# Optimization experiments

Hardware: AMD Instinct MI355X
Metric: run time of the kernel (lower is better)

## Reference

```python
import jax, jax.numpy as jnp
import numpy as np


def setup_inputs() -> dict:
    key = jax.random.key(0)
    ks = jax.random.split(key, 8)
    B, T, U = 4, 256, 128
    De, Dp, D, V = 512, 512, 640, 1024
    s = lambda k, sh, fan: jax.random.normal(k, sh, dtype=jnp.float32) / np.sqrt(fan)
    return {
        "enc": jax.random.normal(ks[0], (B, T, De), dtype=jnp.float32),
        "pred": jax.random.normal(ks[1], (B, U, Dp), dtype=jnp.float32),
        "W_enc": s(ks[2], (De, D), De),
        "b_enc": jnp.zeros((D,), jnp.float32),
        "W_pred": s(ks[3], (Dp, D), Dp),
        "b_pred": jnp.zeros((D,), jnp.float32),
        "W_joint": s(ks[4], (D, V), D),
        "b_joint": jnp.zeros((V,), jnp.float32),
    }


def reference(enc, pred, W_enc, b_enc, W_pred, b_pred, W_joint, b_joint):
    # f: [B,T,D], g: [B,U,D]
    f = jnp.einsum("bte,ed->btd", enc, W_enc) + b_enc
    g = jnp.einsum("bup,pd->bud", pred, W_pred) + b_pred
    # broadcast-add over the T x U lattice, tanh activation
    joint = jnp.tanh(f[:, :, None, :] + g[:, None, :, :])  # [B,T,U,D]
    # final projection to num_classes
    out = jnp.einsum("btud,dv->btuv", joint, W_joint) + b_joint  # [B,T,U,V]
    return out
```

## Files before the change

kernel.cpp:

```cpp
#include <hip/hip_runtime.h>
#include <hip/hip_bf16.h>
#include <stdint.h>

typedef unsigned short u16;
typedef __attribute__((ext_vector_type(8))) __bf16 bf16x8;
typedef __attribute__((ext_vector_type(4))) float f32x4;
typedef __attribute__((ext_vector_type(16))) float f32x16;
typedef __attribute__((ext_vector_type(8))) unsigned short u16x8;
typedef __attribute__((ext_vector_type(4))) unsigned int u32x4;

static __device__ __forceinline__ u16 f2bf(float x) {
  __hip_bfloat16 h = __float2bfloat16(x);
  u16 u;
  __builtin_memcpy(&u, &h, 2);
  return u;
}

static __device__ __forceinline__ float fast_tanh(float x) {
  float e = __expf(2.0f * x);
  return 1.0f - 2.0f * __builtin_amdgcn_rcpf(e + 1.0f);
}

static __device__ __forceinline__ void gload_lds16(const void* g, void* l) {
  __builtin_amdgcn_global_load_lds(
      (const __attribute__((address_space(1))) unsigned int*)g,
      (__attribute__((address_space(3))) unsigned int*)l, 16, 0, 0);
}

static __device__ __forceinline__ int swz(int row, int byte_in_row) {
  return row * 128 + (byte_in_row ^ ((row & 7) << 4));
}

__global__ __launch_bounds__(256) void transpose_cast_kernel(
    const float* __restrict__ in, u16* __restrict__ out, int K, int N) {
  int n = blockIdx.x;
  for (int k = threadIdx.x; k < K; k += 256) {
    out[(size_t)n * K + k] = f2bf(in[(size_t)k * N + n]);
  }
}

__global__ __launch_bounds__(256) void linear_kernel(
    const float* __restrict__ A, const u16* __restrict__ Wt,
    const float* __restrict__ bias, float* __restrict__ out) {
  __shared__ u16 sA[64 * 64];
  __shared__ u16 sB[64 * 64];
  const int t = threadIdx.x;
  const int bx = blockIdx.x;
  const int m0 = (bx / 10) * 64;
  const int n0 = (bx % 10) * 64;
  const int lane = t & 63, wid = t >> 6;
  const int wr = wid >> 1, wc = wid & 1;
  const int l15 = lane & 15, lk8 = (lane >> 4) << 3;

  const int srow = t >> 2;
  const int kc = (t & 3) << 4;

  f32x4 acc[2][2] = {};

  for (int k0 = 0; k0 < 512; k0 += 64) {
    {
      const float4* gp = (const float4*)(A + (size_t)(m0 + srow) * 512 + k0 + kc);
      u16 tmp[16];
#pragma unroll
      for (int i = 0; i < 4; ++i) {
        float4 v = gp[i];
        tmp[i * 4 + 0] = f2bf(v.x);
        tmp[i * 4 + 1] = f2bf(v.y);
        tmp[i * 4 + 2] = f2bf(v.z);
        tmp[i * 4 + 3] = f2bf(v.w);
      }
      *(u16x8*)((char*)sA + swz(srow, kc * 2)) = *(u16x8*)&tmp[0];
      *(u16x8*)((char*)sA + swz(srow, kc * 2 + 16)) = *(u16x8*)&tmp[8];
    }
    {
      const int off = (t & 3) << 5;
      const char* gsrc = (const char*)Wt + ((size_t)(n0 + srow) * 512 + k0) * 2 + off;
      u32x4 q0 = *(const u32x4*)gsrc;
      u32x4 q1 = *(const u32x4*)(gsrc + 16);
      *(u32x4*)((char*)sB + swz(srow, off)) = q0;
      *(u32x4*)((char*)sB + swz(srow, off + 16)) = q1;
    }
    __syncthreads();
#pragma unroll
    for (int kh = 0; kh < 2; ++kh) {
      const int kbyte = kh * 64 + lk8 * 2;
      bf16x8 av[2], bv[2];
#pragma unroll
      for (int mf = 0; mf < 2; ++mf)
        av[mf] = *(const bf16x8*)((char*)sA + swz(wr * 32 + mf * 16 + l15, kbyte));
#pragma unroll
      for (int nf = 0; nf < 2; ++nf)
        bv[nf] = *(const bf16x8*)((char*)sB + swz(wc * 32 + nf * 16 + l15, kbyte));
#pragma unroll
      for (int mf = 0; mf < 2; ++mf)
#pragma unroll
        for (int nf = 0; nf < 2; ++nf)
          acc[mf][nf] = __builtin_amdgcn_mfma_f32_16x16x32_bf16(
              av[mf], bv[nf], acc[mf][nf], 0, 0, 0);
    }
    __syncthreads();
  }

  const int r4 = (lane >> 4) << 2;
#pragma unroll
  for (int nf = 0; nf < 2; ++nf) {
    const int nc = n0 + wc * 32 + nf * 16 + l15;
    const float bjv = bias[nc];
#pragma unroll
    for (int mf = 0; mf < 2; ++mf) {
      const int mr = m0 + wr * 32 + mf * 16 + r4;
#pragma unroll
      for (int r = 0; r < 4; ++r)
        out[(size_t)(mr + r) * 640 + nc] = acc[mf][nf][r] + bjv;
    }
  }
}

__global__ __launch_bounds__(256) void joint_kernel(
    const float* __restrict__ f, const float* __restrict__ g,
    u16* __restrict__ joint, int m_base) {
  int idx = blockIdx.x * 256 + threadIdx.x;
  int row = idx / 80;
  int kc = (idx % 80) * 8;
  int m = m_base + row;
  int bt = m >> 7;
  int b = bt >> 8;
  int u = m & 127;
  const float4* fp = (const float4*)(f + (size_t)bt * 640 + kc);
  const float4* gp = (const float4*)(g + ((size_t)(b * 128 + u)) * 640 + kc);
  u16 tmp[8];
#pragma unroll
  for (int i = 0; i < 2; ++i) {
    float4 fv = fp[i];
    float4 gv = gp[i];
    tmp[i * 4 + 0] = f2bf(fast_tanh(fv.x + gv.x));
    tmp[i * 4 + 1] = f2bf(fast_tanh(fv.y + gv.y));
    tmp[i * 4 + 2] = f2bf(fast_tanh(fv.z + gv.z));
    tmp[i * 4 + 3] = f2bf(fast_tanh(fv.w + gv.w));
  }
  *(u16x8*)(joint + (size_t)row * 640 + kc) = *(u16x8*)&tmp[0];
}

__global__ __launch_bounds__(512, 2) void gemm256_kernel(
    const u16* __restrict__ A,
    const u16* __restrict__ Bt,
    const float* __restrict__ bias,
    float* __restrict__ out,
    int m_base, int mtiles) {
  extern __shared__ char smem[];
  const int t = threadIdx.x;
  const int lane = t & 63, wid = t >> 6;

  const int nwg = mtiles * 4;
  const int bid = blockIdx.x;
  const int q = nwg >> 3, r = nwg & 7;
  const int xcd = bid & 7, local = bid >> 3;
  const int wgid = (xcd < r ? xcd * (q + 1) : r * (q + 1) + (xcd - r) * q) + local;
  const int mt = wgid >> 2, nt = wgid & 3;

  const int wr = wid >> 2, wc = wid & 3;
  const int l31 = lane & 31, hi = lane >> 5;
  const int rx = (lane & 7) << 4;

  const int srow = t >> 3;
  const int xc = ((t & 7) ^ ((t >> 3) & 7)) << 4;
  const u16* aSrc[4];
  const u16* bSrc[4];
#pragma unroll
  for (int j = 0; j < 4; ++j) {
    const int row = j * 64 + srow;
    aSrc[j] = A + (size_t)(mt * 256 + row) * 640 + (xc >> 1);
    bSrc[j] = Bt + (size_t)(nt * 256 + row) * 640 + (xc >> 1);
  }
  const int sdst = wid * 1024;

  f32x16 acc[4][2] = {};

#pragma unroll
  for (int j = 0; j < 4; ++j) {
    gload_lds16(aSrc[j], smem + j * 8192 + sdst);
    gload_lds16(bSrc[j], smem + 32768 + j * 8192 + sdst);
  }
  __syncthreads();

  for (int tt = 0; tt < 10; ++tt) {
    const int bufo = (tt & 1) * 65536;
    if (tt < 9) {
      const int ke = (tt + 1) * 64;
      const int nbufo = bufo ^ 65536;
#pragma unroll
      for (int j = 0; j < 4; ++j) {
        gload_lds16(aSrc[j] + ke, smem + nbufo + j * 8192 + sdst);
        gload_lds16(bSrc[j] + ke, smem + nbufo + 32768 + j * 8192 + sdst);
      }
    }
    const char* sA = smem + bufo;
    const char* sB = smem + bufo + 32768;
#pragma unroll
    for (int ks = 0; ks < 4; ++ks) {
      const int cb = (ks * 32 + (hi << 4)) ^ rx;
      bf16x8 bv[2], av[4];
#pragma unroll
      for (int nn = 0; nn < 2; ++nn)
        bv[nn] = *(const bf16x8*)(sB + (wc * 64 + nn * 32 + l31) * 128 + cb);
#pragma unroll
      for (int mm = 0; mm < 4; ++mm)
        av[mm] = *(const bf16x8*)(sA + (wr * 128 + mm * 32 + l31) * 128 + cb);
      __builtin_amdgcn_s_setprio(1);
#pragma unroll
      for (int mm = 0; mm < 4; ++mm)
#pragma unroll
        for (int nn = 0; nn < 2; ++nn)
          acc[mm][nn] = __builtin_amdgcn_mfma_f32_32x32x16_bf16(
              av[mm], bv[nn], acc[mm][nn], 0, 0, 0);
      __builtin_amdgcn_s_setprio(0);
    }
    if (tt < 9) __syncthreads();
  }

#pragma unroll
  for (int nn = 0; nn < 2; ++nn) {
    const int v = nt * 256 + wc * 64 + nn * 32 + l31;
    const float bjv = bias[v];
#pragma unroll
    for (int mm = 0; mm < 4; ++mm) {
      const size_t mrow =
          (size_t)m_base + (size_t)mt * 256 + wr * 128 + mm * 32 + hi * 4;
#pragma unroll
      for (int reg = 0; reg < 16; ++reg) {
        const int row = (reg & 3) + 8 * (reg >> 2);
        out[(mrow + row) * 1024 + v] = acc[mm][nn][reg] + bjv;
      }
    }
  }
}

__global__ __launch_bounds__(512) void fused_joint_kernel(
    const float* __restrict__ f, const float* __restrict__ g,
    const u16* __restrict__ Wjt, const float* __restrict__ bj,
    float* __restrict__ out) {
  __shared__ u16 sA[128 * 64];
  __shared__ u16 sB[256 * 64];
  const int t = threadIdx.x;
  const int bt = blockIdx.x;
  const int b = bt >> 8;
  const int v0 = blockIdx.y << 8;
  const float* frow = f + (size_t)bt * 640;
  const float* gbase = g + (size_t)b * 128 * 640;

  const int lane = t & 63, wid = t >> 6;
  const int wr = wid >> 2, wc = wid & 3;
  const int l15 = lane & 15, lk8 = (lane >> 4) << 3;

  const int au = t >> 2;
  const int akc = (t & 3) << 4;
  const int bn = t >> 1;
  const int boff = (t & 1) << 6;

  f32x4 acc[4][4] = {};

  for (int k0 = 0; k0 < 640; k0 += 64) {
    {
      const float4* gp = (const float4*)(gbase + (size_t)au * 640 + k0 + akc);
      const float4* fp = (const float4*)(frow + k0 + akc);
      u16 tmp[16];
#pragma unroll
      for (int i = 0; i < 4; ++i) {
        float4 gv = gp[i];
        float4 fv = fp[i];
        tmp[i * 4 + 0] = f2bf(fast_tanh(gv.x + fv.x));
        tmp[i * 4 + 1] = f2bf(fast_tanh(gv.y + fv.y));
        tmp[i * 4 + 2] = f2bf(fast_tanh(gv.z + fv.z));
        tmp[i * 4 + 3] = f2bf(fast_tanh(gv.w + fv.w));
      }
      *(u16x8*)((char*)sA + swz(au, akc * 2)) = *(u16x8*)&tmp[0];
      *(u16x8*)((char*)sA + swz(au, akc * 2 + 16)) = *(u16x8*)&tmp[8];
    }
    {
      const char* gsrc = (const char*)Wjt + ((size_t)(v0 + bn) * 640 + k0) * 2 + boff;
#pragma unroll
      for (int i = 0; i < 4; ++i) {
        u32x4 qv = *(const u32x4*)(gsrc + i * 16);
        *(u32x4*)((char*)sB + swz(bn, boff + i * 16)) = qv;
      }
    }
    __syncthreads();
#pragma unroll
    for (int kh = 0; kh < 2; ++kh) {
      const int kbyte = kh * 64 + lk8 * 2;
      bf16x8 av[4], bv[4];
#pragma unroll
      for (int mf = 0; mf < 4; ++mf)
        av[mf] = *(const bf16x8*)((char*)sA + swz(wr * 64 + mf * 16 + l15, kbyte));
#pragma unroll
      for (int nf = 0; nf < 4; ++nf)
        bv[nf] = *(const bf16x8*)((char*)sB + swz(wc * 64 + nf * 16 + l15, kbyte));
#pragma unroll
      for (int mf = 0; mf < 4; ++mf)
#pragma unroll
        for (int nf = 0; nf < 4; ++nf)
          acc[mf][nf] = __builtin_amdgcn_mfma_f32_16x16x32_bf16(
              av[mf], bv[nf], acc[mf][nf], 0, 0, 0);
    }
    __syncthreads();
  }

  const int r4 = (lane >> 4) << 2;
#pragma unroll
  for (int nf = 0; nf < 4; ++nf) {
    const int v = v0 + wc * 64 + nf * 16 + l15;
    const float bjv = bj[v];
#pragma unroll
    for (int mf = 0; mf < 4; ++mf) {
      const int u = wr * 64 + mf * 16 + r4;
      const size_t o = ((size_t)bt * 128 + u) * 1024 + v;
#pragma unroll
      for (int rr = 0; rr < 4; ++rr)
        out[o + (size_t)rr * 1024] = acc[mf][nf][rr] + bjv;
    }
  }
}

extern "C" void kernel_launch(void* const* d_in, const int* in_sizes, int n_in,
                              void* d_out, int out_size, void* d_ws, size_t ws_size,
                              hipStream_t stream) {
  const float* enc = (const float*)d_in[0];
  const float* pred = (const float*)d_in[1];
  const float* W_enc = (const float*)d_in[2];
  const float* b_enc = (const float*)d_in[3];
  const float* W_pred = (const float*)d_in[4];
  const float* b_pred = (const float*)d_in[5];
  const float* W_joint = (const float*)d_in[6];
  const float* b_joint = (const float*)d_in[7];
  float* out = (float*)d_out;

  char* ws = (char*)d_ws;
  float* f = (float*)ws;
  float* gbuf = (float*)(ws + 2621440);
  u16* Wet = (u16*)(ws + 2621440 + 1310720);
  u16* Wpt = (u16*)(ws + 2621440 + 1310720 + 655360);
  u16* Wjt = (u16*)(ws + 2621440 + 1310720 + 2 * 655360);
  const size_t fixed = 2621440 + 1310720 + 2 * 655360 + 1310720;
  u16* joint = (u16*)(ws + fixed);

  transpose_cast_kernel<<<640, 256, 0, stream>>>(W_enc, Wet, 512, 640);
  transpose_cast_kernel<<<640, 256, 0, stream>>>(W_pred, Wpt, 512, 640);
  transpose_cast_kernel<<<1024, 256, 0, stream>>>(W_joint, Wjt, 640, 1024);

  linear_kernel<<<16 * 10, 256, 0, stream>>>(enc, Wet, b_enc, f);
  linear_kernel<<<8 * 10, 256, 0, stream>>>(pred, Wpt, b_pred, gbuf);

  const long TOTAL_M = 131072;
  long maxrows = ws_size > fixed ? (long)((ws_size - fixed) / 1280) : 0;
  maxrows &= ~255L;

  if (maxrows >= 16384) {
    (void)hipFuncSetAttribute((const void*)gemm256_kernel,
                              hipFuncAttributeMaxDynamicSharedMemorySize, 131072);
    long CH = maxrows >= TOTAL_M ? TOTAL_M : maxrows;
    for (long m0 = 0; m0 < TOTAL_M; m0 += CH) {
      long R = TOTAL_M - m0 < CH ? TOTAL_M - m0 : CH;
      int mtiles = (int)(R / 256);
      joint_kernel<<<(int)(R / 128) * 40, 256, 0, stream>>>(f, gbuf, joint, (int)m0);
      gemm256_kernel<<<mtiles * 4, 512, 131072, stream>>>(joint, Wjt, b_joint, out,
                                                          (int)m0, mtiles);
    }
  } else {
    fused_joint_kernel<<<dim3(1024, 4), 512, 0, stream>>>(f, gbuf, Wjt, b_joint, out);
  }
}
```

Baseline: 342.0 us.

## Shrink joint GEMM tile from 256x256 to 128x128 with 256-thread blocks

```diff
diff --git a/kernel.cpp b/kernel.cpp
--- a/kernel.cpp
+++ b/kernel.cpp
@@ -141,7 +141,7 @@
   *(u16x8*)(joint + (size_t)row * 640 + kc) = *(u16x8*)&tmp[0];
 }
 
-__global__ __launch_bounds__(512, 2) void gemm256_kernel(
+__global__ __launch_bounds__(256, 4) void gemm128_kernel(
     const u16* __restrict__ A,
     const u16* __restrict__ Bt,
     const float* __restrict__ bias,
@@ -151,64 +151,56 @@
   const int t = threadIdx.x;
   const int lane = t & 63, wid = t >> 6;
 
-  const int nwg = mtiles * 4;
+  const int nwg = mtiles * 8;
   const int bid = blockIdx.x;
-  const int q = nwg >> 3, r = nwg & 7;
+  const int q = nwg >> 3;
   const int xcd = bid & 7, local = bid >> 3;
-  const int wgid = (xcd < r ? xcd * (q + 1) : r * (q + 1) + (xcd - r) * q) + local;
-  const int mt = wgid >> 2, nt = wgid & 3;
-
-  const int wr = wid >> 2, wc = wid & 3;
+  const int wgid = xcd * q + local;
+  const int mt = wgid >> 3, nt = wgid & 7;
+
+  const size_t a0 = (size_t)mt * 128 * 640;
+  const int n0 = nt * 128;
+
+  const int wr = wid >> 1, wc = wid & 1;
   const int l31 = lane & 31, hi = lane >> 5;
   const int rx = (lane & 7) << 4;
 
-  const int srow = t >> 3;
-  const int xc = ((t & 7) ^ ((t >> 3) & 7)) << 4;
-  const u16* aSrc[4];
-  const u16* bSrc[4];
-#pragma unroll
-  for (int j = 0; j < 4; ++j) {
-    const int row = j * 64 + srow;
-    aSrc[j] = A + (size_t)(mt * 256 + row) * 640 + (xc >> 1);
-    bSrc[j] = Bt + (size_t)(nt * 256 + row) * 640 + (xc >> 1);
-  }
-  const int sdst = wid * 1024;
-
-  f32x16 acc[4][2] = {};
-
-#pragma unroll
-  for (int j = 0; j < 4; ++j) {
-    gload_lds16(aSrc[j], smem + j * 8192 + sdst);
-    gload_lds16(bSrc[j], smem + 32768 + j * 8192 + sdst);
-  }
+  const int srow = lane >> 3;
+  const int scol = (((lane & 7) ^ (lane >> 3)) << 3);
+
+  f32x16 acc[2][2] = {};
+
+#define STAGE(k0, nb)                                                        \
+  _Pragma("unroll") for (int j = 0; j < 4; ++j) {                            \
+    const int i_ = wid * 4 + j;                                              \
+    const int row_ = i_ * 8 + srow;                                          \
+    gload_lds16(A + a0 + (size_t)row_ * 640 + (k0) + scol,                   \
+                smem + (nb) + i_ * 1024);                                    \
+    gload_lds16(Bt + (size_t)(n0 + row_) * 640 + (k0) + scol,                \
+                smem + (nb) + 16384 + i_ * 1024);                            \
+  }
+
+  STAGE(0, 0)
   __syncthreads();
 
   for (int tt = 0; tt < 10; ++tt) {
-    const int bufo = (tt & 1) * 65536;
-    if (tt < 9) {
-      const int ke = (tt + 1) * 64;
-      const int nbufo = bufo ^ 65536;
-#pragma unroll
-      for (int j = 0; j < 4; ++j) {
-        gload_lds16(aSrc[j] + ke, smem + nbufo + j * 8192 + sdst);
-        gload_lds16(bSrc[j] + ke, smem + nbufo + 32768 + j * 8192 + sdst);
-      }
-    }
+    const int bufo = (tt & 1) * 32768;
+    if (tt < 9) STAGE((tt + 1) * 64, bufo ^ 32768)
     const char* sA = smem + bufo;
-    const char* sB = smem + bufo + 32768;
+    const char* sB = smem + bufo + 16384;
 #pragma unroll
     for (int ks = 0; ks < 4; ++ks) {
       const int cb = (ks * 32 + (hi << 4)) ^ rx;
-      bf16x8 bv[2], av[4];
+      bf16x8 av[2], bv[2];
+#pragma unroll
+      for (int mm = 0; mm < 2; ++mm)
+        av[mm] = *(const bf16x8*)(sA + (wr * 64 + mm * 32 + l31) * 128 + cb);
 #pragma unroll
       for (int nn = 0; nn < 2; ++nn)
         bv[nn] = *(const bf16x8*)(sB + (wc * 64 + nn * 32 + l31) * 128 + cb);
-#pragma unroll
-      for (int mm = 0; mm < 4; ++mm)
-        av[mm] = *(const bf16x8*)(sA + (wr * 128 + mm * 32 + l31) * 128 + cb);
       __builtin_amdgcn_s_setprio(1);
 #pragma unroll
-      for (int mm = 0; mm < 4; ++mm)
+      for (int mm = 0; mm < 2; ++mm)
 #pragma unroll
         for (int nn = 0; nn < 2; ++nn)
           acc[mm][nn] = __builtin_amdgcn_mfma_f32_32x32x16_bf16(
@@ -217,15 +209,16 @@
     }
     if (tt < 9) __syncthreads();
   }
+#undef STAGE
 
 #pragma unroll
   for (int nn = 0; nn < 2; ++nn) {
-    const int v = nt * 256 + wc * 64 + nn * 32 + l31;
+    const int v = n0 + wc * 64 + nn * 32 + l31;
     const float bjv = bias[v];
 #pragma unroll
-    for (int mm = 0; mm < 4; ++mm) {
+    for (int mm = 0; mm < 2; ++mm) {
       const size_t mrow =
-          (size_t)m_base + (size_t)mt * 256 + wr * 128 + mm * 32 + hi * 4;
+          (size_t)m_base + (size_t)mt * 128 + wr * 64 + mm * 32 + hi * 4;
 #pragma unroll
       for (int reg = 0; reg < 16; ++reg) {
         const int row = (reg & 3) + 8 * (reg >> 2);
@@ -352,18 +345,18 @@
 
   const long TOTAL_M = 131072;
   long maxrows = ws_size > fixed ? (long)((ws_size - fixed) / 1280) : 0;
-  maxrows &= ~255L;
+  maxrows &= ~127L;
 
   if (maxrows >= 16384) {
-    (void)hipFuncSetAttribute((const void*)gemm256_kernel,
-                              hipFuncAttributeMaxDynamicSharedMemorySize, 131072);
+    (void)hipFuncSetAttribute((const void*)gemm128_kernel,
+                              hipFuncAttributeMaxDynamicSharedMemorySize, 65536);
     long CH = maxrows >= TOTAL_M ? TOTAL_M : maxrows;
     for (long m0 = 0; m0 < TOTAL_M; m0 += CH) {
       long R = TOTAL_M - m0 < CH ? TOTAL_M - m0 : CH;
-      int mtiles = (int)(R / 256);
-      joint_kernel<<<(int)(R / 128) * 40, 256, 0, stream>>>(f, gbuf, joint, (int)m0);
-      gemm256_kernel<<<mtiles * 4, 512, 131072, stream>>>(joint, Wjt, b_joint, out,
-                                                          (int)m0, mtiles);
+      int mtiles = (int)(R / 128);
+      joint_kernel<<<mtiles * 40, 256, 0, stream>>>(f, gbuf, joint, (int)m0);
+      gemm128_kernel<<<mtiles * 8, 256, 65536, stream>>>(joint, Wjt, b_joint, out,
+                                                         (int)m0, mtiles);
     }
   } else {
     fused_joint_kernel<<<dim3(1024, 4), 512, 0, stream>>>(f, gbuf, Wjt, b_joint, out);
```

New measurement: 392.6 us. +14.8%, slower.
